# Performance work log

Hardware: AMD Instinct MI355X
Metric: run time of the kernel (lower is better)

The kernel has to match this reference:

```python
import jax, jax.numpy as jnp
import numpy as np

B, L, D, NH, K, R = 2, 1024, 768, 12, 24, 768
HD = D // NH            # head_dim = 64
NFFT = 2048             # nearest power of two >= 2*L-1


def _spectral_filters():
    # Hankel matrix Z_{ij} = 2 / ((i+j)^3 - (i+j)), top-K eigvecs scaled by sigma^{1/4}
    e = np.arange(1, L + 1, dtype=np.float64)
    ipj = e[:, None] + e[None, :]
    Z = 2.0 / (ipj ** 3 - ipj)
    sigma, phi = np.linalg.eigh(Z)
    phi_k = phi[:, -K:] * (sigma[-K:] ** 0.25)
    return jnp.asarray(phi_k, dtype=jnp.float32)  # (L, K)


def setup_inputs() -> dict:
    key = jax.random.key(0)
    ks = jax.random.split(key, 16)
    s = 0.02
    lin = lambda k_, i, o: jax.random.normal(k_, (i, o), jnp.float32) * s
    return {
        "x": jax.random.normal(ks[0], (B, L, D), jnp.float32),
        "stu_filters": _spectral_filters(),
        "M_inputs": jax.random.normal(ks[1], (D, R), jnp.float32) * s,
        "M_filters": jax.random.normal(ks[2], (K, R), jnp.float32) * s,
        "wq_w": lin(ks[3], D, D), "wq_b": jnp.zeros((D,), jnp.float32),
        "wk_w": lin(ks[4], D, D), "wk_b": jnp.zeros((D,), jnp.float32),
        "wv_w": lin(ks[5], D, D), "wv_b": jnp.zeros((D,), jnp.float32),
        "wg_w": lin(ks[6], D, D), "wg_b": jnp.zeros((D,), jnp.float32),
        "wo_w": lin(ks[7], D, D), "wo_b": jnp.zeros((D,), jnp.float32),
    }


def _stu_features(x, stu_filters, M_inputs, M_filters):
    # tensordot STU path: project inputs and filters to rank R, then FFT causal conv
    u = x @ M_inputs                       # (B, L, R)
    phi = stu_filters @ M_filters          # (L, R)
    sgn = jnp.where(jnp.arange(L) % 2 == 0, 1.0, -1.0)[None, :, None]  # (1, L, 1)
    V = jnp.fft.rfft(phi, n=NFFT, axis=0)  # (NFFT//2+1, R)
    U = jnp.stack([u, u * sgn], axis=-1)   # (B, L, R, 2)
    Uf = jnp.fft.rfft(U, n=NFFT, axis=1)   # (B, NFFT//2+1, R, 2)
    conv = jnp.fft.irfft(V[None, :, :, None] * Uf, n=NFFT, axis=1)[:, :L]  # (B, L, R, 2)
    u_plus = conv[..., 0]
    u_minus = conv[..., 1] * sgn
    return u_plus + u_minus               # (B, L, R) with R == D


def reference(x, stu_filters, M_inputs, M_filters,
              wq_w, wq_b, wk_w, wk_b, wv_w, wv_b,
              wg_w, wg_b, wo_w, wo_b):
    x_tilde = _stu_features(x, stu_filters, M_inputs, M_filters)  # (B, L, D)

    heads = lambda y: y.reshape(B, L, NH, HD).transpose(0, 2, 1, 3)  # (B, H, L, h)
    q = heads(x @ wq_w + wq_b)
    k = heads(x @ wk_w + wk_b)
    v = heads(x @ wv_w + wv_b)

    # causal linear attention via cumulative outer-product state
    Z = jnp.einsum('bhtp,bhtn->bhtpn', v, k)     # (B, H, L, h, h)
    Hc = jnp.cumsum(Z, axis=2)
    Y = jnp.einsum('bhtp,bhtpn->bhtn', q, Hc)    # (B, H, L, h)
    y_attn = Y.transpose(0, 2, 1, 3).reshape(B, L, D)

    gate = jax.nn.sigmoid(x @ wg_w + wg_b)
    y = x_tilde + (y_attn - x_tilde) * gate
    return y @ wo_w + wo_b
```

## Files before the change

### kernel.cpp

```cpp
#include <hip/hip_runtime.h>
#include <math.h>

#define B_  2
#define L_  1024
#define D_  768
#define NH_ 12
#define HD_ 64
#define K_  24
#define R_  768
#define NC_ 16
#define CS_ 64

typedef __bf16 bf16x8 __attribute__((ext_vector_type(8)));
typedef float f32x4 __attribute__((ext_vector_type(4)));
typedef unsigned short u16x8 __attribute__((ext_vector_type(8)));

__device__ inline unsigned short f2bf(float f) {
    union { float f; unsigned u; } v; v.f = f;
    unsigned r = v.u + 0x7FFFu + ((v.u >> 16) & 1u);
    return (unsigned short)(r >> 16);
}

__device__ inline ushort4 pack4(const f32x4 v) {
    ushort4 r;
    r.x = f2bf(v[0]); r.y = f2bf(v[1]); r.z = f2bf(v[2]); r.w = f2bf(v[3]);
    return r;
}

#define GLD_LDS16(g, l)                                                     \
    __builtin_amdgcn_global_load_lds(                                       \
        (const __attribute__((address_space(1))) void*)(g),                 \
        (__attribute__((address_space(3))) void*)(l), 16, 0, 0)

__global__ __launch_bounds__(256) void k_prep(const float* __restrict__ w0,
                                              const float* __restrict__ w1,
                                              const float* __restrict__ w2,
                                              const float* __restrict__ w3,
                                              const float* __restrict__ w4,
                                              const float* __restrict__ w5,
                                              unsigned short* __restrict__ Wt,
                                              const float* __restrict__ x,
                                              unsigned short* __restrict__ xb,
                                              const float* __restrict__ F,
                                              const float* __restrict__ Mf,
                                              float* __restrict__ phi2) {
    const int bid = blockIdx.x;
    const int tid = threadIdx.x;
    if (bid < 864) {
        const int z = bid / 144, rem = bid % 144;
        const float* W;
        switch (z) {
            case 0: W = w0; break;
            case 1: W = w1; break;
            case 2: W = w2; break;
            case 3: W = w3; break;
            case 4: W = w4; break;
            default: W = w5; break;
        }
        unsigned short* o = Wt + (size_t)z * D_ * D_;
        __shared__ float t[64][65];
        const int n0 = (rem % 12) * 64, k0 = (rem / 12) * 64;
        const int c = tid & 63, rq = tid >> 6;
#pragma unroll
        for (int i = 0; i < 16; ++i)
            t[rq + i * 4][c] = W[(size_t)(k0 + rq + i * 4) * D_ + n0 + c];
        __syncthreads();
#pragma unroll
        for (int i = 0; i < 16; ++i)
            o[(size_t)(n0 + rq + i * 4) * D_ + k0 + c] = f2bf(t[c][rq + i * 4]);
    } else if (bid < 1632) {
        const int i8 = ((bid - 864) * 256 + tid) * 8;
        float4 f0 = *reinterpret_cast<const float4*>(x + i8);
        float4 f1 = *reinterpret_cast<const float4*>(x + i8 + 4);
        u16x8 p;
        p[0] = f2bf(f0.x); p[1] = f2bf(f0.y); p[2] = f2bf(f0.z); p[3] = f2bf(f0.w);
        p[4] = f2bf(f1.x); p[5] = f2bf(f1.y); p[6] = f2bf(f1.z); p[7] = f2bf(f1.w);
        *reinterpret_cast<u16x8*>(xb + i8) = p;
    } else {
        const int idx = (bid - 1632) * 256 + tid;
        const int r = idx % R_;
        const int j = idx / R_;
        float acc = 0.f;
#pragma unroll
        for (int kk = 0; kk < K_; ++kk)
            acc += F[j * K_ + kk] * Mf[kk * R_ + r];
        phi2[idx] = 2.f * acc;
    }
}

template <int NBF>
__device__ __forceinline__ void gemm_core(const unsigned short* __restrict__ A,
                                          const unsigned short* __restrict__ Bt,
                                          const float* __restrict__ bias,
                                          int mode,
                                          float* __restrict__ cf,
                                          unsigned short* __restrict__ cbf,
                                          unsigned short* __restrict__ ct,
                                          int N, int Kd,
                                          int bm, int bn, int tid) {
    __shared__ unsigned short As[128 * 64];
    __shared__ unsigned short Bs[NBF * 32 * 64];
    const int lane = tid & 63, wave = tid >> 6;
    const int wm = (wave >> 1) * 64, wn = (wave & 1) * (NBF * 16);
    const int l15 = lane & 15, lg = lane >> 4;

    f32x4 acc[4][NBF] = {};

    const int nt = Kd / 64;
    for (int t = 0; t < nt; ++t) {
        const int k0 = t * 64;
        __syncthreads();
#pragma unroll
        for (int q = 0; q < 4; ++q) {
            const int s = q * 256 + tid;
            GLD_LDS16(A + (size_t)(bm + (s >> 3)) * Kd + k0 + (s & 7) * 8,
                      &As[s * 8]);
        }
#pragma unroll
        for (int q = 0; q < NBF; ++q) {
            const int s = q * 256 + tid;
            GLD_LDS16(Bt + (size_t)(bn + (s >> 3)) * Kd + k0 + (s & 7) * 8,
                      &Bs[s * 8]);
        }
        __syncthreads();
#pragma unroll
        for (int ks = 0; ks < 2; ++ks) {
            const int kb = ks * 32 + lg * 8;
            bf16x8 a[4], b[NBF];
#pragma unroll
            for (int f = 0; f < 4; ++f)
                a[f] = *reinterpret_cast<const bf16x8*>(
                    &As[(wm + f * 16 + l15) * 64 + kb]);
#pragma unroll
            for (int f = 0; f < NBF; ++f)
                b[f] = *reinterpret_cast<const bf16x8*>(
                    &Bs[(wn + f * 16 + l15) * 64 + kb]);
#pragma unroll
            for (int fm = 0; fm < 4; ++fm)
#pragma unroll
                for (int fn = 0; fn < NBF; ++fn)
                    acc[fm][fn] = __builtin_amdgcn_mfma_f32_16x16x32_bf16(
                        a[fm], b[fn], acc[fm][fn], 0, 0, 0);
        }
    }

#pragma unroll
    for (int fm = 0; fm < 4; ++fm)
#pragma unroll
        for (int fn = 0; fn < NBF; ++fn) {
            const int col = bn + wn + fn * 16 + l15;
            const float bv = bias ? bias[col] : 0.f;
            const int r0 = bm + wm + fm * 16 + lg * 4;
            f32x4 v = acc[fm][fn];
            v[0] += bv; v[1] += bv; v[2] += bv; v[3] += bv;
            if (mode == 0) {
#pragma unroll
                for (int j = 0; j < 4; ++j)
                    cf[(size_t)(r0 + j) * N + col] = v[j];
            }
            if (mode & 1) {
#pragma unroll
                for (int j = 0; j < 4; ++j)
                    cbf[(size_t)(r0 + j) * D_ + col] = f2bf(v[j]);
            }
            if (mode & 2) {
                const int h = col >> 6, n = col & 63;
                const int bI = r0 >> 10, l0 = r0 & 1023;
                *reinterpret_cast<ushort4*>(
                    ct + (((size_t)bI * NH_ + h) * 64 + n) * (size_t)L_ + l0) =
                    pack4(v);
            }
        }
}

__global__ __launch_bounds__(256) void k_gemm(const unsigned short* __restrict__ A,
                                              const unsigned short* __restrict__ Bt,
                                              const float* __restrict__ bias,
                                              float* __restrict__ C,
                                              int N, int Kd) {
    gemm_core<2>(A, Bt, bias, 0, C, nullptr, nullptr, N, Kd,
                 blockIdx.y * 128, blockIdx.x * 64, threadIdx.x);
}

__global__ __launch_bounds__(256) void k_gemm5(const unsigned short* __restrict__ A,
                                               const unsigned short* __restrict__ wt,
                                               const float* __restrict__ bq,
                                               const float* __restrict__ bk,
                                               const float* __restrict__ bv,
                                               const float* __restrict__ bg,
                                               float* __restrict__ ubuf,
                                               unsigned short* __restrict__ qbf,
                                               unsigned short* __restrict__ ktb,
                                               unsigned short* __restrict__ vbf,
                                               unsigned short* __restrict__ vtb,
                                               float* __restrict__ gb) {
    const int z = blockIdx.z;
    const float* bias = nullptr;
    int mode = 0;
    float* cf = nullptr; unsigned short* cbf = nullptr; unsigned short* ct = nullptr;
    switch (z) {
        case 0: mode = 0; cf = ubuf; bias = nullptr; break;
        case 1: mode = 1; cbf = qbf; bias = bq; break;
        case 2: mode = 2; ct = ktb; bias = bk; break;
        case 3: mode = 3; cbf = vbf; ct = vtb; bias = bv; break;
        default: mode = 0; cf = gb; bias = bg; break;
    }
    const unsigned short* Bt = wt + (size_t)z * D_ * D_;
    gemm_core<4>(A, Bt, bias, mode, cf, cbf, ct, D_, D_,
                 blockIdx.y * 128, blockIdx.x * 128, threadIdx.x);
}

__global__ __launch_bounds__(768) void k_conv(const float* __restrict__ u,
                                              const float* __restrict__ phi2,
                                              float* __restrict__ xt) {
    __shared__ f32x4 red[4][8][192];
    const int tid = threadIdx.x;
    const int g   = tid / 192;
    const int lr  = tid % 192;
    const int r   = lr * 4;
    const int m0  = blockIdx.x * 8;
    const int bp  = blockIdx.y;
    const int b   = bp >> 1, p = bp & 1;

    f32x4 acc[8] = {};
    f32x4 w[8]   = {};

    const int ns = g * 128;
    const int ne = min(ns + 128, m0 + 8);

    if (ns < ne) {
        if (g > 0) {
#pragma unroll
            for (int j = 1; j <= 7; ++j)
                w[(8 - j) & 7] =
                    *reinterpret_cast<const f32x4*>(phi2 + (size_t)(2 * (ns - j)) * R_ + r);
        }
        const float* pp = phi2 + (size_t)(2 * ns) * R_ + r;
        const float* up = u + ((size_t)(b * L_) + (size_t)(2 * (m0 + 7 - ns) + p)) * R_ + r;
        for (int i = ns; i < ne; i += 8) {
#pragma unroll
            for (int k = 0; k < 8; ++k) {
                const f32x4 wn = *reinterpret_cast<const f32x4*>(pp);
                const f32x4 un = *reinterpret_cast<const f32x4*>(up);
                w[k] = wn;
#pragma unroll
                for (int a = 0; a < 8; ++a)
                    acc[a] += w[(k + a + 1) & 7] * un;
                pp += 2 * R_;
                up -= 2 * R_;
            }
        }
    }

#pragma unroll
    for (int a = 0; a < 8; ++a) red[g][a][lr] = acc[a];
    __syncthreads();

#pragma unroll
    for (int q2 = 0; q2 < 2; ++q2) {
        const int sl = q2 * 768 + tid;
        const int a  = sl / 192, l = sl % 192;
        const f32x4 s = red[0][a][l] + red[1][a][l] + red[2][a][l] + red[3][a][l];
        *reinterpret_cast<f32x4*>(
            xt + ((size_t)(b * L_) + (size_t)(2 * (m0 + a) + p)) * R_ + l * 4) = s;
    }
}

__global__ __launch_bounds__(256) void k_attn(const unsigned short* __restrict__ qbf,
                                              const unsigned short* __restrict__ vbf,
                                              const unsigned short* __restrict__ ktb,
                                              const unsigned short* __restrict__ vtb,
                                              const float* __restrict__ xt,
                                              const float* __restrict__ g,
                                              unsigned short* __restrict__ gx) {
    const int c = blockIdx.x, h = blockIdx.y, b = blockIdx.z;
    __shared__ unsigned short Qs[64 * 64];
    __shared__ unsigned short Vs[64 * 64];
    __shared__ unsigned short Kc[64 * 64];
    __shared__ unsigned short Tk[64 * 64];
    __shared__ unsigned short Tv[64 * 64];
    __shared__ unsigned short Sl[64 * 72];
    __shared__ unsigned short Hl[64 * 72];

    const int tid = threadIdx.x;
    const int lane = tid & 63, wave = tid >> 6;
    const int wr = (wave >> 1) * 32, wc = (wave & 1) * 32;
    const int l15 = lane & 15, lg = lane >> 4;

    {
        const size_t rowbase = ((size_t)(b * L_ + c * CS_)) * D_ + h * HD_;
        const size_t tbase = ((size_t)(b * NH_ + h)) * 64 * (size_t)L_ + c * 64;
#pragma unroll
        for (int q2 = 0; q2 < 2; ++q2) {
            const int s = q2 * 256 + tid;
            const int row = s >> 3, c8 = s & 7;
            GLD_LDS16(qbf + rowbase + (size_t)row * D_ + c8 * 8, &Qs[s * 8]);
            GLD_LDS16(vbf + rowbase + (size_t)row * D_ + c8 * 8, &Vs[s * 8]);
            GLD_LDS16(ktb + tbase + (size_t)row * L_ + c8 * 8, &Kc[s * 8]);
        }
    }

    f32x4 hacc[2][2] = {};
    for (int cc = 0; cc < c; ++cc) {
        __syncthreads();
        const size_t tb2 = ((size_t)(b * NH_ + h)) * 64 * (size_t)L_ + cc * 64;
#pragma unroll
        for (int q2 = 0; q2 < 2; ++q2) {
            const int s = q2 * 256 + tid;
            const int row = s >> 3, c8 = s & 7;
            GLD_LDS16(ktb + tb2 + (size_t)row * L_ + c8 * 8, &Tk[s * 8]);
            GLD_LDS16(vtb + tb2 + (size_t)row * L_ + c8 * 8, &Tv[s * 8]);
        }
        __syncthreads();
#pragma unroll
        for (int ks = 0; ks < 2; ++ks) {
            const int kb = ks * 32 + lg * 8;
            bf16x8 av[2], bk[2];
#pragma unroll
            for (int f = 0; f < 2; ++f) {
                av[f] = *reinterpret_cast<const bf16x8*>(&Tv[(wr + f * 16 + l15) * 64 + kb]);
                bk[f] = *reinterpret_cast<const bf16x8*>(&Tk[(wc + f * 16 + l15) * 64 + kb]);
            }
#pragma unroll
            for (int fm = 0; fm < 2; ++fm)
#pragma unroll
                for (int fn = 0; fn < 2; ++fn)
                    hacc[fm][fn] = __builtin_amdgcn_mfma_f32_16x16x32_bf16(
                        av[fm], bk[fn], hacc[fm][fn], 0, 0, 0);
        }
    }
    __syncthreads();

    if (c > 0) {
#pragma unroll
        for (int fm = 0; fm < 2; ++fm)
#pragma unroll
            for (int fn = 0; fn < 2; ++fn) {
                const int n = wc + fn * 16 + l15;
                const int p0 = wr + fm * 16 + lg * 4;
                *reinterpret_cast<ushort4*>(&Hl[n * 72 + p0]) = pack4(hacc[fm][fn]);
            }
    }

    {
        f32x4 sacc[2][2] = {};
#pragma unroll
        for (int ks = 0; ks < 2; ++ks) {
            const int kb = ks * 32 + lg * 8;
            bf16x8 av[2], bq[2];
#pragma unroll
            for (int f = 0; f < 2; ++f) {
                av[f] = *reinterpret_cast<const bf16x8*>(&Vs[(wr + f * 16 + l15) * 64 + kb]);
                bq[f] = *reinterpret_cast<const bf16x8*>(&Qs[(wc + f * 16 + l15) * 64 + kb]);
            }
#pragma unroll
            for (int fm = 0; fm < 2; ++fm)
#pragma unroll
                for (int fn = 0; fn < 2; ++fn)
                    sacc[fm][fn] = __builtin_amdgcn_mfma_f32_16x16x32_bf16(
                        av[fm], bq[fn], sacc[fm][fn], 0, 0, 0);
        }
#pragma unroll
        for (int fm = 0; fm < 2; ++fm)
#pragma unroll
            for (int fn = 0; fn < 2; ++fn) {
                const int t = wc + fn * 16 + l15;
                const int s0 = wr + fm * 16 + lg * 4;
#pragma unroll
                for (int j = 0; j < 4; ++j)
                    if (s0 + j > t) sacc[fm][fn][j] = 0.f;
                *reinterpret_cast<ushort4*>(&Sl[t * 72 + s0]) = pack4(sacc[fm][fn]);
            }
    }
    __syncthreads();

    f32x4 yacc[2][2] = {};
#pragma unroll
    for (int ks = 0; ks < 2; ++ks) {
        const int kb = ks * 32 + lg * 8;
        bf16x8 ak[2], bs[2];
#pragma unroll
        for (int f = 0; f < 2; ++f) {
            ak[f] = *reinterpret_cast<const bf16x8*>(&Kc[(wr + f * 16 + l15) * 64 + kb]);
            bs[f] = *reinterpret_cast<const bf16x8*>(&Sl[(wc + f * 16 + l15) * 72 + kb]);
        }
#pragma unroll
        for (int fm = 0; fm < 2; ++fm)
#pragma unroll
            for (int fn = 0; fn < 2; ++fn)
                yacc[fm][fn] = __builtin_amdgcn_mfma_f32_16x16x32_bf16(
                    ak[fm], bs[fn], yacc[fm][fn], 0, 0, 0);
    }
    if (c > 0) {
#pragma unroll
        for (int ks = 0; ks < 2; ++ks) {
            const int kb = ks * 32 + lg * 8;
            bf16x8 ah[2], bq[2];
#pragma unroll
            for (int f = 0; f < 2; ++f) {
                ah[f] = *reinterpret_cast<const bf16x8*>(&Hl[(wr + f * 16 + l15) * 72 + kb]);
                bq[f] = *reinterpret_cast<const bf16x8*>(&Qs[(wc + f * 16 + l15) * 64 + kb]);
            }
#pragma unroll
            for (int fm = 0; fm < 2; ++fm)
#pragma unroll
                for (int fn = 0; fn < 2; ++fn)
                    yacc[fm][fn] = __builtin_amdgcn_mfma_f32_16x16x32_bf16(
                        ah[fm], bq[fn], yacc[fm][fn], 0, 0, 0);
        }
    }

#pragma unroll
    for (int fm = 0; fm < 2; ++fm)
#pragma unroll
        for (int fn = 0; fn < 2; ++fn) {
            const int n0 = wr + fm * 16 + lg * 4;
            const int t = wc + fn * 16 + l15;
            const size_t idx = ((size_t)(b * L_ + c * CS_ + t)) * D_ + h * HD_ + n0;
            const float4 gv = *reinterpret_cast<const float4*>(g + idx);
            const float4 xv = *reinterpret_cast<const float4*>(xt + idx);
            f32x4 y = yacc[fm][fn];
            ushort4 o;
            {
                const float s0 = 1.f / (1.f + expf(-gv.x));
                o.x = f2bf(xv.x + (y[0] - xv.x) * s0);
                const float s1 = 1.f / (1.f + expf(-gv.y));
                o.y = f2bf(xv.y + (y[1] - xv.y) * s1);
                const float s2 = 1.f / (1.f + expf(-gv.z));
                o.z = f2bf(xv.z + (y[2] - xv.z) * s2);
                const float s3 = 1.f / (1.f + expf(-gv.w));
                o.w = f2bf(xv.w + (y[3] - xv.w) * s3);
            }
            *reinterpret_cast<ushort4*>(gx + idx) = o;
        }
}

extern "C" void kernel_launch(void* const* d_in, const int* in_sizes, int n_in,
                              void* d_out, int out_size, void* d_ws, size_t ws_size,
                              hipStream_t stream) {
    const float* x    = (const float*)d_in[0];
    const float* stu  = (const float*)d_in[1];
    const float* Mi   = (const float*)d_in[2];
    const float* Mf   = (const float*)d_in[3];
    const float* wq_w = (const float*)d_in[4];
    const float* wq_b = (const float*)d_in[5];
    const float* wk_w = (const float*)d_in[6];
    const float* wk_b = (const float*)d_in[7];
    const float* wv_w = (const float*)d_in[8];
    const float* wv_b = (const float*)d_in[9];
    const float* wg_w = (const float*)d_in[10];
    const float* wg_b = (const float*)d_in[11];
    const float* wo_w = (const float*)d_in[12];
    const float* wo_b = (const float*)d_in[13];
    float* out = (float*)d_out;

    char* ws = (char*)d_ws;
    size_t o = 0;
    const size_t WSZ = (size_t)D_ * D_;
    unsigned short* wbf = (unsigned short*)(ws + o); o += 6 * WSZ * 2;
    unsigned short* xbf = (unsigned short*)(ws + o); o += (size_t)B_ * L_ * D_ * 2;
    unsigned short* gx  = (unsigned short*)(ws + o); o += (size_t)B_ * L_ * D_ * 2;
    unsigned short* qbf = (unsigned short*)(ws + o); o += (size_t)B_ * L_ * D_ * 2;
    unsigned short* vbf = (unsigned short*)(ws + o); o += (size_t)B_ * L_ * D_ * 2;
    unsigned short* ktb = (unsigned short*)(ws + o); o += (size_t)B_ * NH_ * 64 * L_ * 2;
    unsigned short* vtb = (unsigned short*)(ws + o); o += (size_t)B_ * NH_ * 64 * L_ * 2;
    float* ubuf = (float*)(ws + o); o += (size_t)B_ * L_ * R_ * 4;
    float* phi2 = (float*)(ws + o); o += (size_t)L_ * R_ * 4;
    float* xt   = (float*)(ws + o); o += (size_t)B_ * L_ * R_ * 4;
    float* gb   = (float*)(ws + o); o += (size_t)B_ * L_ * D_ * 4;

    unsigned short* wo_t = wbf + 5 * WSZ;

    const dim3 blk(256);

    k_prep<<<dim3(4704), blk, 0, stream>>>(Mi, wq_w, wk_w, wv_w, wg_w, wo_w, wbf,
                                           x, xbf, stu, Mf, phi2);

    k_gemm5<<<dim3(D_ / 128, (B_ * L_) / 128, 5), blk, 0, stream>>>(
        xbf, wbf, wq_b, wk_b, wv_b, wg_b, ubuf, qbf, ktb, vbf, vtb, gb);

    k_conv<<<dim3(L_ / 2 / 8, B_ * 2), dim3(768), 0, stream>>>(ubuf, phi2, xt);

    k_attn<<<dim3(NC_, NH_, B_), blk, 0, stream>>>(qbf, vbf, ktb, vtb, xt, gb, gx);

    k_gemm<<<dim3(D_ / 64, (B_ * L_) / 128), blk, 0, stream>>>(gx, wo_t, wo_b, out, D_, D_);
}
```

Baseline: 109.2 us.

## Double-buffer GEMM LDS tiles and shrink output-projection tile to 64x64

```diff
diff --git a/kernel.cpp b/kernel.cpp
--- a/kernel.cpp
+++ b/kernel.cpp
@@ -88,7 +88,7 @@
     }
 }
 
-template <int NBF>
+template <int FM, int FN>
 __device__ __forceinline__ void gemm_core(const unsigned short* __restrict__ A,
                                           const unsigned short* __restrict__ Bt,
                                           const float* __restrict__ bias,
@@ -98,56 +98,64 @@
                                           unsigned short* __restrict__ ct,
                                           int N, int Kd,
                                           int bm, int bn, int tid) {
-    __shared__ unsigned short As[128 * 64];
-    __shared__ unsigned short Bs[NBF * 32 * 64];
+    constexpr int BM = 2 * FM * 16;
+    constexpr int BN = 2 * FN * 16;
+    __shared__ unsigned short As[2][BM * 64];
+    __shared__ unsigned short Bs[2][BN * 64];
     const int lane = tid & 63, wave = tid >> 6;
-    const int wm = (wave >> 1) * 64, wn = (wave & 1) * (NBF * 16);
+    const int wm = (wave >> 1) * (FM * 16), wn = (wave & 1) * (FN * 16);
     const int l15 = lane & 15, lg = lane >> 4;
 
-    f32x4 acc[4][NBF] = {};
-
+    f32x4 acc[FM][FN] = {};
+
+    auto stage = [&](int buf, int k0) {
+#pragma unroll
+        for (int q = 0; q < FM; ++q) {
+            const int s = q * 256 + tid;
+            GLD_LDS16(A + (size_t)(bm + (s >> 3)) * Kd + k0 + (s & 7) * 8,
+                      &As[buf][s * 8]);
+        }
+#pragma unroll
+        for (int q = 0; q < FN; ++q) {
+            const int s = q * 256 + tid;
+            GLD_LDS16(Bt + (size_t)(bn + (s >> 3)) * Kd + k0 + (s & 7) * 8,
+                      &Bs[buf][s * 8]);
+        }
+    };
+
+    stage(0, 0);
+    __syncthreads();
+    int cur = 0;
     const int nt = Kd / 64;
     for (int t = 0; t < nt; ++t) {
-        const int k0 = t * 64;
-        __syncthreads();
-#pragma unroll
-        for (int q = 0; q < 4; ++q) {
-            const int s = q * 256 + tid;
-            GLD_LDS16(A + (size_t)(bm + (s >> 3)) * Kd + k0 + (s & 7) * 8,
-                      &As[s * 8]);
-        }
-#pragma unroll
-        for (int q = 0; q < NBF; ++q) {
-            const int s = q * 256 + tid;
-            GLD_LDS16(Bt + (size_t)(bn + (s >> 3)) * Kd + k0 + (s & 7) * 8,
-                      &Bs[s * 8]);
-        }
-        __syncthreads();
+        if (t + 1 < nt) stage(cur ^ 1, (t + 1) * 64);
 #pragma unroll
         for (int ks = 0; ks < 2; ++ks) {
             const int kb = ks * 32 + lg * 8;
-            bf16x8 a[4], b[NBF];
-#pragma unroll
-            for (int f = 0; f < 4; ++f)
+            bf16x8 a[FM], b[FN];
+#pragma unroll
+            for (int f = 0; f < FM; ++f)
                 a[f] = *reinterpret_cast<const bf16x8*>(
-                    &As[(wm + f * 16 + l15) * 64 + kb]);
-#pragma unroll
-            for (int f = 0; f < NBF; ++f)
+                    &As[cur][(wm + f * 16 + l15) * 64 + kb]);
+#pragma unroll
+            for (int f = 0; f < FN; ++f)
                 b[f] = *reinterpret_cast<const bf16x8*>(
-                    &Bs[(wn + f * 16 + l15) * 64 + kb]);
-#pragma unroll
-            for (int fm = 0; fm < 4; ++fm)
-#pragma unroll
-                for (int fn = 0; fn < NBF; ++fn)
+                    &Bs[cur][(wn + f * 16 + l15) * 64 + kb]);
+#pragma unroll
+            for (int fm = 0; fm < FM; ++fm)
+#pragma unroll
+                for (int fn = 0; fn < FN; ++fn)
                     acc[fm][fn] = __builtin_amdgcn_mfma_f32_16x16x32_bf16(
                         a[fm], b[fn], acc[fm][fn], 0, 0, 0);
         }
-    }
-
-#pragma unroll
-    for (int fm = 0; fm < 4; ++fm)
-#pragma unroll
-        for (int fn = 0; fn < NBF; ++fn) {
+        __syncthreads();
+        cur ^= 1;
+    }
+
+#pragma unroll
+    for (int fm = 0; fm < FM; ++fm)
+#pragma unroll
+        for (int fn = 0; fn < FN; ++fn) {
             const int col = bn + wn + fn * 16 + l15;
             const float bv = bias ? bias[col] : 0.f;
             const int r0 = bm + wm + fm * 16 + lg * 4;
@@ -178,8 +186,8 @@
                                               const float* __restrict__ bias,
                                               float* __restrict__ C,
                                               int N, int Kd) {
-    gemm_core<2>(A, Bt, bias, 0, C, nullptr, nullptr, N, Kd,
-                 blockIdx.y * 128, blockIdx.x * 64, threadIdx.x);
+    gemm_core<2, 2>(A, Bt, bias, 0, C, nullptr, nullptr, N, Kd,
+                    blockIdx.y * 64, blockIdx.x * 64, threadIdx.x);
 }
 
 __global__ __launch_bounds__(256) void k_gemm5(const unsigned short* __restrict__ A,
@@ -206,8 +214,8 @@
         default: mode = 0; cf = gb; bias = bg; break;
     }
     const unsigned short* Bt = wt + (size_t)z * D_ * D_;
-    gemm_core<4>(A, Bt, bias, mode, cf, cbf, ct, D_, D_,
-                 blockIdx.y * 128, blockIdx.x * 128, threadIdx.x);
+    gemm_core<4, 4>(A, Bt, bias, mode, cf, cbf, ct, D_, D_,
+                    blockIdx.y * 128, blockIdx.x * 128, threadIdx.x);
 }
 
 __global__ __launch_bounds__(768) void k_conv(const float* __restrict__ u,
@@ -483,5 +491,5 @@
 
     k_attn<<<dim3(NC_, NH_, B_), blk, 0, stream>>>(qbf, vbf, ktb, vtb, xt, gb, gx);
 
-    k_gemm<<<dim3(D_ / 64, (B_ * L_) / 128), blk, 0, stream>>>(gx, wo_t, wo_b, out, D_, D_);
-}
+    k_gemm<<<dim3(D_ / 64, (B_ * L_) / 64), blk, 0, stream>>>(gx, wo_t, wo_b, out, D_, D_);
+}
```

Result: faster. 100.0 us (-8.4%).
